# Performance work log

Hardware: AMD Instinct MI355X
Metric: run time of the kernel (lower is better)

## Reference

```python
import jax, jax.numpy as jnp
import numpy as np
from jax import lax

B, C, H, W = 8, 1024, 32, 32
M = 16384
K = 9  # n_neighbors (min(9, M))
NOISE_MIN, NOISE_MAX = 0.01, 0.5
EPS = 1e-08


def setup_inputs() -> dict:
    key = jax.random.key(0)
    k1, k2, k3 = jax.random.split(key, 3)
    features = jax.random.normal(k1, (B, C, H, W), dtype=jnp.float32)
    memory_bank = jax.random.normal(k2, (M, C), dtype=jnp.float32)
    noise = jax.random.normal(k3, (B * H * W, C), dtype=jnp.float32)
    return {"features": features, "memory_bank": memory_bank, "noise": noise}


def _adaptive_noise(features, memory_bank, noise):
    b, c, h, w = features.shape
    # [B,C,H,W] -> [N, C] with N = B*H*W (matches permute(0,2,3,1).reshape(-1,C))
    f = jnp.transpose(features, (0, 2, 3, 1)).reshape(-1, c)

    # influence is computed under torch.no_grad() -> stop gradients here
    fs = lax.stop_gradient(f)
    mb = lax.stop_gradient(memory_bank)

    f_sq = jnp.sum(fs * fs, axis=1, keepdims=True)            # [N,1]
    m_sq = jnp.sum(mb * mb, axis=1)[None, :]                  # [1,M]
    cross = fs @ mb.T                                         # [N,M] GEMM (hot path)
    dist_sq = jnp.maximum(f_sq + m_sq - 2.0 * cross, 0.0)
    distances = jnp.sqrt(dist_sq + EPS)                       # [N,M]

    # top-K smallest distances
    neg_topk, knn_idx = lax.top_k(-distances, K)              # [N,K]
    knn_dist = -neg_topk

    nearest = mb[knn_idx[:, 0]]                               # [N,C]
    d0 = knn_dist[:, 0:1] + EPS                               # [N,1]
    influence = jnp.abs((fs - nearest) / d0)                  # [N,C]
    influence_per_pos = influence.mean(axis=1)                # [N]

    imin = influence_per_pos.min()
    imax = influence_per_pos.max()
    denom = imax - imin
    influence_norm = jnp.where(
        denom > EPS,
        (influence_per_pos - imin) / jnp.maximum(denom, EPS),
        jnp.zeros_like(influence_per_pos),
    )

    noise_std = NOISE_MIN + influence_norm * (NOISE_MAX - NOISE_MIN)  # [N]
    noised_flat = f + noise * noise_std[:, None]

    noised = jnp.transpose(noised_flat.reshape(b, h, w, c), (0, 3, 1, 2))
    influence_map = influence_norm.reshape(b, h, w)
    noise_std_map = noise_std.reshape(b, h, w)
    return noised, influence_map, noise_std_map


def reference(features, memory_bank, noise):
    return _adaptive_noise(features, memory_bank, noise)
```

## Files before the change

kernel.cpp:

```cpp
#include <hip/hip_runtime.h>
#include <stdint.h>
#include <stddef.h>

typedef unsigned short u16;
typedef unsigned int u32;
typedef unsigned long long u64;
typedef __attribute__((ext_vector_type(4))) int i32x4;
typedef __attribute__((ext_vector_type(4))) float f32x4;

#define NPOS 8192
#define MROW 16384
#define CDIM 1024
#define QS 25.4f

__device__ __forceinline__ u32 fkey(float f){
  union { float f; u32 u; } z; z.f = f;
  u32 b = z.u;
  return b ^ ((b & 0x80000000u) ? 0xffffffffu : 0x80000000u);
}
__device__ __forceinline__ float unfkey(u32 u){
  u32 b = (u & 0x80000000u) ? (u ^ 0x80000000u) : ~u;
  union { u32 u; float f; } z; z.u = b; return z.f;
}
__device__ __forceinline__ u64 umin64(u64 a, u64 b){ return a < b ? a : b; }
__device__ __forceinline__ u64 umax64(u64 a, u64 b){ return a > b ? a : b; }
__device__ __forceinline__ float wave_sum(float v){
  #pragma unroll
  for(int o = 32; o; o >>= 1) v += __shfl_xor(v, o, 64);
  return v;
}
__device__ __forceinline__ int q8(float x){
  float y = fminf(fmaxf(x * QS, -127.f), 127.f);
  return __float2int_rn(y) & 0xff;
}

__device__ __forceinline__ void gload16(const void* g, void* l){
  __builtin_amdgcn_global_load_lds((const __attribute__((address_space(1))) u32*)g,
                                   (__attribute__((address_space(3))) u32*)l, 16, 0, 0);
}

__global__ __launch_bounds__(256) void k_prep(const float* __restrict__ mb, const float* __restrict__ feat,
                                              signed char* __restrict__ mq, signed char* __restrict__ fq,
                                              float* __restrict__ fT, float* __restrict__ m_sq,
                                              u32* __restrict__ minmax){
  __shared__ float tile[64][65];
  int bid = blockIdx.x, t = threadIdx.x;
  if(bid < 4096){
    int lane = t & 63, w = t >> 6;
    int row = bid * 4 + w;
    if(row == 0 && lane == 0){ minmax[0] = 0x7f800000u; minmax[1] = 0u; }
    const float4* src = (const float4*)(mb + (size_t)row * CDIM);
    u32* dst = (u32*)(mq + (size_t)row * CDIM);
    float s = 0.f;
    #pragma unroll
    for(int ch = 0; ch < 4; ch++){
      float4 v = src[ch * 64 + lane];
      u32 packed = (u32)q8(v.x) | ((u32)q8(v.y) << 8) | ((u32)q8(v.z) << 16) | ((u32)q8(v.w) << 24);
      dst[ch * 64 + lane] = packed;
      s += v.x*v.x + v.y*v.y + v.z*v.z + v.w*v.w;
    }
    s = wave_sum(s);
    if(lane == 0) m_sq[row] = s;
  } else {
    int e = bid - 4096;
    int b = e >> 8, c0 = ((e >> 4) & 15) * 64, hw0 = (e & 15) * 64;
    int a = t & 63, g = t >> 6;
    const float* fb = feat + ((size_t)b * CDIM + c0) * 1024 + hw0;
    #pragma unroll 4
    for(int r = 0; r < 16; r++){
      int cL = r * 4 + g;
      tile[cL][a] = fb[(size_t)cL * 1024 + a];
    }
    __syncthreads();
    #pragma unroll 4
    for(int r = 0; r < 16; r++){
      int hwL = r * 4 + g;
      int n = b * 1024 + hw0 + hwL;
      int c = c0 + a;
      float x = tile[a][hwL];
      fT[(size_t)n * CDIM + c] = x;
      fq[(size_t)n * CDIM + c] = (signed char)(q8(x) << 24 >> 24);
    }
  }
}

__device__ __forceinline__ i32x4 mfma_i8(i32x4 a, i32x4 b, i32x4 c){
  return __builtin_amdgcn_mfma_i32_16x16x64_i8(a, b, c, 0, 0, 0);
}

__global__ __launch_bounds__(512, 2) void k_gemm(const signed char* __restrict__ fq, const signed char* __restrict__ mq,
                                                 const float* __restrict__ m_sq, u64* __restrict__ cand){
  __shared__ unsigned char lds[4][2][256][64];
  int bid = blockIdx.x;
  int ct = (bid & 7) * 8 + ((bid >> 3) & 7);
  int rt = bid >> 6;
  int t = threadIdx.x, lane = t & 63, wid = t >> 6;
  int wm = wid >> 2, wn = wid & 3;
  int fr = lane & 15, kg = lane >> 4;
  int sr = t >> 2, sl = t & 3;

  int ssw = (sl ^ ((sr >> 1) & 3)) * 16;
  const signed char* pA0 = fq + (size_t)(rt * 256 + sr)       * CDIM + ssw;
  const signed char* pA1 = fq + (size_t)(rt * 256 + sr + 128) * CDIM + ssw;
  const signed char* pB0 = mq + (size_t)(ct * 256 + sr)       * CDIM + ssw;
  const signed char* pB1 = mq + (size_t)(ct * 256 + sr + 128) * CDIM + ssw;
  unsigned char* Ld = &lds[0][0][sr][sl * 16];
  int fsw = (kg ^ ((fr >> 1) & 3)) * 16;
  const unsigned char* La = &lds[0][0][wm * 128 + fr][fsw];
  const unsigned char* Lb = &lds[0][1][wn * 64  + fr][fsw];

  const i32x4 zero = {0, 0, 0, 0};
  i32x4 acc[8][4];
  #pragma unroll
  for(int i = 0; i < 8; i++)
    #pragma unroll
    for(int j = 0; j < 4; j++) acc[i][j] = zero;

#define STAGE(BUF) do{ \
    gload16(pA0, Ld + (BUF) * 32768);                  \
    gload16(pA1, Ld + (BUF) * 32768 + 8192);           \
    gload16(pB0, Ld + (BUF) * 32768 + 16384);          \
    gload16(pB1, Ld + (BUF) * 32768 + 16384 + 8192);   \
    pA0 += 64; pA1 += 64; pB0 += 64; pB1 += 64;        \
  }while(0)

#define COMPUTE(BUF) do{ \
    i32x4 fb[4]; \
    _Pragma("unroll") for(int ni_ = 0; ni_ < 4; ni_++) \
      fb[ni_] = *(const i32x4*)(Lb + (BUF) * 32768 + ni_ * 1024); \
    _Pragma("unroll") for(int mi_ = 0; mi_ < 8; mi_++){ \
      i32x4 fa = *(const i32x4*)(La + (BUF) * 32768 + mi_ * 1024); \
      _Pragma("unroll") for(int ni_ = 0; ni_ < 4; ni_++) \
        acc[mi_][ni_] = mfma_i8(fa, fb[ni_], acc[mi_][ni_]); \
    } \
  }while(0)

#define SYNCV(N) asm volatile("s_waitcnt vmcnt(" #N ") lgkmcnt(0)\n\ts_barrier" ::: "memory")

  STAGE(0); STAGE(1); STAGE(2);
  for(int it = 0; it < 3; ++it){
    SYNCV(8); STAGE(3); COMPUTE(0);
    SYNCV(8); STAGE(0); COMPUTE(1);
    SYNCV(8); STAGE(1); COMPUTE(2);
    SYNCV(8); STAGE(2); COMPUTE(3);
  }
  SYNCV(8); STAGE(3); COMPUTE(0);
  SYNCV(8); COMPUTE(1);
  SYNCV(4); COMPUTE(2);
  SYNCV(0); COMPUTE(3);

#undef STAGE
#undef COMPUTE
#undef SYNCV

  const float SI = 2.0f / (QS * QS);
  float msq[4];
  #pragma unroll
  for(int ni = 0; ni < 4; ni++) msq[ni] = m_sq[ct * 256 + wn * 64 + ni * 16 + fr];
  __syncthreads();
  u64* rl = (u64*)&lds[0][0][0][0];
  #pragma unroll
  for(int mi = 0; mi < 8; mi++){
    #pragma unroll
    for(int j = 0; j < 4; j++){
      u64 k1 = ~0ull, k2 = ~0ull;
      #pragma unroll
      for(int ni = 0; ni < 4; ni++){
        float v = msq[ni] - SI * (float)acc[mi][ni][j];
        u64 key = ((u64)fkey(v) << 32) | (u32)(ct * 256 + wn * 64 + ni * 16 + fr);
        if(key < k1){ k2 = k1; k1 = key; } else if(key < k2){ k2 = key; }
      }
      #pragma unroll
      for(int m = 1; m < 16; m <<= 1){
        u64 o1 = __shfl_xor(k1, m, 64), o2 = __shfl_xor(k2, m, 64);
        u64 n1 = umin64(k1, o1);
        u64 n2 = umin64(umax64(k1, o1), umin64(k2, o2));
        k1 = n1; k2 = n2;
      }
      if(fr == 0){
        int rowl = wm * 128 + mi * 16 + kg * 4 + j;
        rl[(wn * 256 + rowl) * 2 + 0] = k1;
        rl[(wn * 256 + rowl) * 2 + 1] = k2;
      }
    }
  }
  __syncthreads();
  if(t < 256){
    u64 a1 = rl[t * 2], a2 = rl[t * 2 + 1];
    #pragma unroll
    for(int w = 1; w < 4; w++){
      u64 b1 = rl[(w * 256 + t) * 2], b2 = rl[(w * 256 + t) * 2 + 1];
      u64 n1 = umin64(a1, b1);
      u64 n2 = umin64(umax64(a1, b1), umin64(a2, b2));
      a1 = n1; a2 = n2;
    }
    size_t base = ((size_t)(rt * 256 + t)) * 128 + ct * 2;
    cand[base] = a1; cand[base + 1] = a2;
  }
}

__global__ __launch_bounds__(256) void k_finalize(const u64* __restrict__ cand,
    const float* __restrict__ fT,
    const float* __restrict__ mb, const float* __restrict__ m_sq,
    float* __restrict__ inf_arr, u32* __restrict__ minmax){
  int t = threadIdx.x, lane = t & 63, w = t >> 6;
  int n = blockIdx.x * 4 + w;
  const u64* cr = cand + (size_t)n * 128;
  u64 a = cr[lane * 2], b = cr[lane * 2 + 1];
  u64 k1 = umin64(a, b), k2 = umax64(a, b);
  #pragma unroll
  for(int m = 1; m < 64; m <<= 1){
    u64 o1 = __shfl_xor(k1, m, 64), o2 = __shfl_xor(k2, m, 64);
    u64 n1 = umin64(k1, o1);
    u64 n2 = umin64(umax64(k1, o1), umin64(k2, o2));
    k1 = n1; k2 = n2;
  }
  float v1 = unfkey((u32)(k1 >> 32)), v2 = unfkey((u32)(k2 >> 32));
  bool needm = (v2 - v1) <= 10.0f;
  u32 cols[4];
  cols[0] = (u32)k1;
  int nr = 1;
  if(needm){
    nr = 4;
    u64 l1 = umin64(a, b), l2 = umax64(a, b);
    #pragma unroll
    for(int it = 0; it < 4; it++){
      u64 mn = l1;
      #pragma unroll
      for(int m = 1; m < 64; m <<= 1){ u64 o = __shfl_xor(mn, m, 64); mn = umin64(mn, o); }
      cols[it] = (u32)mn;
      if(l1 == mn){ l1 = l2; l2 = ~0ull; }
    }
  }

  float fv[16];
  {
    const float4* fp = (const float4*)(fT + (size_t)n * CDIM) + lane * 4;
    #pragma unroll
    for(int q = 0; q < 4; q++){
      float4 v = fp[q];
      fv[q*4+0] = v.x; fv[q*4+1] = v.y; fv[q*4+2] = v.z; fv[q*4+3] = v.w;
    }
  }
  float fs = 0.f;
  #pragma unroll
  for(int j = 0; j < 16; j++) fs += fv[j] * fv[j];
  fs = wave_sum(fs);

  float bestd = 1e30f; int bestc = 0x7fffffff;
  for(int i = 0; i < nr; ++i){
    int c = (int)cols[i];
    const float4* mrow = (const float4*)(mb + (size_t)c * CDIM) + lane * 4;
    float p = 0.f;
    #pragma unroll
    for(int q = 0; q < 4; q++){
      float4 mv = mrow[q];
      p += fv[q*4+0]*mv.x + fv[q*4+1]*mv.y + fv[q*4+2]*mv.z + fv[q*4+3]*mv.w;
    }
    p = wave_sum(p);
    float d = sqrtf(fmaxf(fs + m_sq[c] - 2.f * p, 0.f) + 1e-8f);
    if(d < bestd || (d == bestd && c < bestc)){ bestd = d; bestc = c; }
  }
  {
    const float4* mrow = (const float4*)(mb + (size_t)bestc * CDIM) + lane * 4;
    float pa = 0.f;
    #pragma unroll
    for(int q = 0; q < 4; q++){
      float4 mv = mrow[q];
      pa += fabsf(fv[q*4+0]-mv.x) + fabsf(fv[q*4+1]-mv.y) + fabsf(fv[q*4+2]-mv.z) + fabsf(fv[q*4+3]-mv.w);
    }
    pa = wave_sum(pa);
    if(lane == 0){
      float inf = pa / (1024.0f * (bestd + 1e-8f));
      inf_arr[n] = inf;
      atomicMin(&minmax[0], __float_as_uint(inf));
      atomicMax(&minmax[1], __float_as_uint(inf));
    }
  }
}

__global__ __launch_bounds__(256) void k_noise(const float* __restrict__ feat, const float* __restrict__ noise,
                                               const float* __restrict__ inf_arr, const u32* __restrict__ minmax,
                                               float* __restrict__ out){
  __shared__ float tile[64][65];
  __shared__ float ns[64];
  int b = blockIdx.z, c0 = blockIdx.y * 64, hw0 = blockIdx.x * 64;
  int t = threadIdx.x, a = t & 63, g = t >> 6;
  if(t < 64){
    int n = b * 1024 + hw0 + t;
    float imin = __uint_as_float(minmax[0]);
    float imax = __uint_as_float(minmax[1]);
    float denom = imax - imin;
    float x = inf_arr[n];
    float norm = (denom > 1e-8f) ? ((x - imin) / fmaxf(denom, 1e-8f)) : 0.0f;
    float nsv = 0.01f + norm * 0.49f;
    ns[t] = nsv;
    if(c0 == 0){
      out[8388608 + n] = norm;
      out[8396800 + n] = nsv;
    }
  }
  #pragma unroll 4
  for(int r = 0; r < 16; r++){
    int j = r * 4 + g;
    tile[a][j] = noise[((size_t)(b * 1024 + hw0 + j)) * CDIM + c0 + a];
  }
  __syncthreads();
  #pragma unroll 4
  for(int r = 0; r < 16; r++){
    int i = r * 4 + g;
    size_t idx = ((size_t)b * CDIM + c0 + i) * 1024 + hw0 + a;
    out[idx] = feat[idx] + tile[i][a] * ns[a];
  }
}

extern "C" void kernel_launch(void* const* d_in, const int* in_sizes, int n_in,
                              void* d_out, int out_size, void* d_ws, size_t ws_size,
                              hipStream_t stream){
  const float* features = (const float*)d_in[0];
  const float* mb       = (const float*)d_in[1];
  const float* noise    = (const float*)d_in[2];
  float* out = (float*)d_out;
  char* ws = (char*)d_ws;

  float* fT = (float*)d_out;

  size_t off = 0;
  signed char* mq = (signed char*)(ws + off); off += (size_t)MROW * CDIM;
  signed char* fq = (signed char*)(ws + off); off += (size_t)NPOS * CDIM;
  float* m_sq    = (float*)(ws + off); off += (size_t)MROW * 4;
  float* inf_arr = (float*)(ws + off); off += (size_t)NPOS * 4;
  u32* minmax    = (u32*)(ws + off);   off += 256;
  u64* cand      = (u64*)(ws + off);   off += (size_t)NPOS * 128 * 8;

  k_prep<<<4096 + 2048, 256, 0, stream>>>(mb, features, mq, fq, fT, m_sq, minmax);
  k_gemm<<<dim3(2048), 512, 0, stream>>>(fq, mq, m_sq, cand);
  k_finalize<<<2048, 256, 0, stream>>>(cand, fT, mb, m_sq, inf_arr, minmax);
  k_noise<<<dim3(16, 16, 8), 256, 0, stream>>>(features, noise, inf_arr, minmax, out);
}
```

Measured before the change: 471.3 us.

## Vectorize transpose kernels and shrink GEMM pipeline to double buffering

The feature transpose/quantize kernel and the noise kernel now move data with float4 loads and stores and packed int8 writes, where they previously used scalar accesses, to cut memory instruction count. The int8 GEMM drops its 4-stage LDS ring for a 2-stage double buffer with full vmcnt(0) waits. This halves the GEMM's LDS footprint, which could allow more resident blocks, but exposes global load latency at every barrier. The float4 LDS transposes may also cause bank conflicts.

```diff
diff --git a/kernel.cpp b/kernel.cpp
--- a/kernel.cpp
+++ b/kernel.cpp
@@ -64,22 +64,27 @@
   } else {
     int e = bid - 4096;
     int b = e >> 8, c0 = ((e >> 4) & 15) * 64, hw0 = (e & 15) * 64;
-    int a = t & 63, g = t >> 6;
-    const float* fb = feat + ((size_t)b * CDIM + c0) * 1024 + hw0;
     #pragma unroll 4
-    for(int r = 0; r < 16; r++){
-      int cL = r * 4 + g;
-      tile[cL][a] = fb[(size_t)cL * 1024 + a];
+    for(int r = 0; r < 4; r++){
+      int li = r * 256 + t;
+      int cL = li >> 4, q = li & 15;
+      float4 v = *((const float4*)(feat + ((size_t)b * CDIM + c0 + cL) * 1024 + hw0) + q);
+      tile[cL][q * 4 + 0] = v.x; tile[cL][q * 4 + 1] = v.y;
+      tile[cL][q * 4 + 2] = v.z; tile[cL][q * 4 + 3] = v.w;
     }
     __syncthreads();
     #pragma unroll 4
-    for(int r = 0; r < 16; r++){
-      int hwL = r * 4 + g;
+    for(int r = 0; r < 4; r++){
+      int li = r * 256 + t;
+      int hwL = li >> 4, q = li & 15;
+      float4 v;
+      v.x = tile[q * 4 + 0][hwL]; v.y = tile[q * 4 + 1][hwL];
+      v.z = tile[q * 4 + 2][hwL]; v.w = tile[q * 4 + 3][hwL];
       int n = b * 1024 + hw0 + hwL;
-      int c = c0 + a;
-      float x = tile[a][hwL];
-      fT[(size_t)n * CDIM + c] = x;
-      fq[(size_t)n * CDIM + c] = (signed char)(q8(x) << 24 >> 24);
+      int c = c0 + q * 4;
+      *((float4*)(fT + (size_t)n * CDIM + c)) = v;
+      u32 packed = (u32)q8(v.x) | ((u32)q8(v.y) << 8) | ((u32)q8(v.z) << 16) | ((u32)q8(v.w) << 24);
+      *((u32*)(fq + (size_t)n * CDIM + c)) = packed;
     }
   }
 }
@@ -90,7 +95,7 @@
 
 __global__ __launch_bounds__(512, 2) void k_gemm(const signed char* __restrict__ fq, const signed char* __restrict__ mq,
                                                  const float* __restrict__ m_sq, u64* __restrict__ cand){
-  __shared__ unsigned char lds[4][2][256][64];
+  __shared__ unsigned char lds[2][2][256][64];
   int bid = blockIdx.x;
   int ct = (bid & 7) * 8 + ((bid >> 3) & 7);
   int rt = bid >> 6;
@@ -135,23 +140,20 @@
     } \
   }while(0)
 
-#define SYNCV(N) asm volatile("s_waitcnt vmcnt(" #N ") lgkmcnt(0)\n\ts_barrier" ::: "memory")
-
-  STAGE(0); STAGE(1); STAGE(2);
-  for(int it = 0; it < 3; ++it){
-    SYNCV(8); STAGE(3); COMPUTE(0);
-    SYNCV(8); STAGE(0); COMPUTE(1);
-    SYNCV(8); STAGE(1); COMPUTE(2);
-    SYNCV(8); STAGE(2); COMPUTE(3);
-  }
-  SYNCV(8); STAGE(3); COMPUTE(0);
-  SYNCV(8); COMPUTE(1);
-  SYNCV(4); COMPUTE(2);
-  SYNCV(0); COMPUTE(3);
+#define SYNC0() asm volatile("s_waitcnt vmcnt(0) lgkmcnt(0)\n\ts_barrier" ::: "memory")
+
+  STAGE(0);
+  SYNC0();
+  for(int it = 0; it < 7; ++it){
+    STAGE(1); COMPUTE(0); SYNC0();
+    STAGE(0); COMPUTE(1); SYNC0();
+  }
+  STAGE(1); COMPUTE(0); SYNC0();
+  COMPUTE(1);
 
 #undef STAGE
 #undef COMPUTE
-#undef SYNCV
+#undef SYNC0
 
   const float SI = 2.0f / (QS * QS);
   float msq[4];
@@ -285,7 +287,7 @@
   __shared__ float tile[64][65];
   __shared__ float ns[64];
   int b = blockIdx.z, c0 = blockIdx.y * 64, hw0 = blockIdx.x * 64;
-  int t = threadIdx.x, a = t & 63, g = t >> 6;
+  int t = threadIdx.x;
   if(t < 64){
     int n = b * 1024 + hw0 + t;
     float imin = __uint_as_float(minmax[0]);
@@ -301,16 +303,26 @@
     }
   }
   #pragma unroll 4
-  for(int r = 0; r < 16; r++){
-    int j = r * 4 + g;
-    tile[a][j] = noise[((size_t)(b * 1024 + hw0 + j)) * CDIM + c0 + a];
+  for(int r = 0; r < 4; r++){
+    int li = r * 256 + t;
+    int j = li >> 4, q = li & 15;
+    float4 v = *((const float4*)(noise + ((size_t)(b * 1024 + hw0 + j)) * CDIM + c0) + q);
+    tile[q * 4 + 0][j] = v.x; tile[q * 4 + 1][j] = v.y;
+    tile[q * 4 + 2][j] = v.z; tile[q * 4 + 3][j] = v.w;
   }
   __syncthreads();
   #pragma unroll 4
-  for(int r = 0; r < 16; r++){
-    int i = r * 4 + g;
-    size_t idx = ((size_t)b * CDIM + c0 + i) * 1024 + hw0 + a;
-    out[idx] = feat[idx] + tile[i][a] * ns[a];
+  for(int r = 0; r < 4; r++){
+    int li = r * 256 + t;
+    int i = li >> 4, h4 = li & 15;
+    size_t idx = ((size_t)b * CDIM + c0 + i) * 1024 + hw0 + h4 * 4;
+    float4 f = *(const float4*)(feat + idx);
+    float4 o;
+    o.x = f.x + tile[i][h4 * 4 + 0] * ns[h4 * 4 + 0];
+    o.y = f.y + tile[i][h4 * 4 + 1] * ns[h4 * 4 + 1];
+    o.z = f.z + tile[i][h4 * 4 + 2] * ns[h4 * 4 + 2];
+    o.w = f.w + tile[i][h4 * 4 + 3] * ns[h4 * 4 + 3];
+    *(float4*)(out + idx) = o;
   }
 }
 
```

Measured after the change: 473.6 us. Within noise of the previous version (+0.5%).
